# Optimization experiments

Measured on AMD Instinct MI355X. Metric: run time of the kernel, lower is better.

The kernel has to match this reference:

```python
import jax, jax.numpy as jnp
import numpy as np

HEADDIM = 128
CHUNK = 256


def _ssd_scan(x, dt, A, B, C, chunk):
    # x: (b,l,h,p)  dt: (b,l,h)  A: (h,)  B,C: (b,l,n)  (single group g=1 shared by all heads)
    b, l, h, p = x.shape
    n = B.shape[-1]
    nc = l // chunk
    dA = dt * A  # (b,l,h)
    xc = x.reshape(b, nc, chunk, h, p)
    dtc = dt.reshape(b, nc, chunk, h)
    dAc = dA.reshape(b, nc, chunk, h)
    Bc = B.reshape(b, nc, chunk, n)
    Cc = C.reshape(b, nc, chunk, n)
    cs = jnp.cumsum(dAc, axis=2)  # (b,nc,c,h) cumulative log-decay within chunk
    # intra-chunk quadratic part
    CB = jnp.einsum('bjin,bjkn->bjik', Cc, Bc)  # (b,nc,c,c)
    decay = jnp.exp(cs[:, :, :, None, :] - cs[:, :, None, :, :])  # (b,nc,i,k,h)
    mask = jnp.tril(jnp.ones((chunk, chunk), dtype=bool))
    decay = jnp.where(mask[None, None, :, :, None], decay, 0.0)
    y_intra = jnp.einsum('bjik,bjikh,bjkh,bjkhp->bjihp', CB, decay, dtc, xc)
    # per-chunk end states
    decay_states = jnp.exp(cs[:, :, -1:, :] - cs)  # (b,nc,c,h)
    states = jnp.einsum('bjkh,bjkh,bjkn,bjkhp->bjhnp', decay_states, dtc, Bc, xc)
    # recurrence across chunks: h_j = exp(sum dA_j) * h_{j-1} + states_j
    chunk_decay = jnp.exp(cs[:, :, -1, :])  # (b,nc,h)
    def step(carry, inp):
        s, d = inp
        new = carry * d[:, :, None, None] + s
        return new, carry  # emit state BEFORE this chunk
    init = jnp.zeros((b, h, n, p), x.dtype)
    _, prev = jax.lax.scan(step, init,
                           (states.transpose(1, 0, 2, 3, 4), chunk_decay.transpose(1, 0, 2)))
    prev = prev.transpose(1, 0, 2, 3, 4)  # (b,nc,h,n,p)
    y_inter = jnp.einsum('bjih,bjin,bjhnp->bjihp', jnp.exp(cs), Cc, prev)
    return (y_intra + y_inter).reshape(b, l, h, p)


def setup_inputs() -> dict:
    key = jax.random.key(0)
    k1, k2, k3, k4 = jax.random.split(key, 4)
    b, l, d_inner, nheads, d_state = 2, 4096, 2048, 16, 256
    x = jax.random.normal(k1, (b, l, d_inner), dtype=jnp.float32)
    BC = jax.random.normal(k2, (b, l, 2 * d_state), dtype=jnp.float32) * 0.1
    dt = jax.random.normal(k3, (b, l, 2 * nheads), dtype=jnp.float32) - 3.0
    A_log = jnp.zeros((nheads,), dtype=jnp.float32)
    D = jnp.ones((nheads,), dtype=jnp.float32)
    W_fcD = jax.random.normal(k4, (nheads, d_inner), dtype=jnp.float32) * 0.02
    return {"x": x, "BC": BC, "dt": dt, "A_log": A_log, "D": D, "W_fcD": W_fcD}


def reference(x, BC, dt, A_log, D, W_fcD):
    b, l, dim = x.shape
    h = A_log.shape[0]
    p = HEADDIM
    d_state = BC.shape[-1] // 2
    A = -jnp.exp(A_log)
    # bidirectional: concat forward stream with time-flipped backward stream along batch
    dt2 = jnp.concatenate((dt[:, :, :h], jnp.flip(dt[:, :, h:], axis=1)), axis=0)
    dt2 = jax.nn.softplus(dt2)
    x_og = x
    x2 = jnp.concatenate((x, jnp.flip(x, axis=1)), axis=0)
    BC2 = jnp.concatenate((BC, jnp.flip(BC, axis=1)), axis=0)
    B, C = BC2[..., :d_state], BC2[..., d_state:]
    y = _ssd_scan(x2.reshape(2 * b, l, h, p), dt2, A, B, C, CHUNK)
    y = y.reshape(2 * b, l, dim)
    y = jnp.roll(y, shift=1, axis=1).at[:, 0, :].set(0.0)
    y_fw, y_bw = y[:b], jnp.flip(y[b:], axis=1)
    gate = x_og @ W_fcD.T + D  # (b,l,h)
    y = y_fw + y_bw + x_og * jnp.repeat(gate, p, axis=-1)
    return y
```

## Files before the change

### kernel.cpp

```cpp
#include <hip/hip_runtime.h>
#include <stdint.h>

#define NB 2
#define SL 4096
#define NH 16
#define HD 128
#define DS 256
#define CK 256
#define NCH 16
#define NSQ 4
#define DI 2048

typedef unsigned short u16;
typedef unsigned int u32;
typedef __attribute__((ext_vector_type(8))) __bf16 bf16x8;
typedef __attribute__((ext_vector_type(4))) float f32x4;

__device__ __forceinline__ int tor(int dir, int t) { return dir ? (SL - 1 - t) : t; }

__device__ __forceinline__ u16 f2bf(float f) {
  u32 u = __float_as_uint(f);
  u = u + 0x7fffu + ((u >> 16) & 1u);
  return (u16)(u >> 16);
}
__device__ __forceinline__ float bf2f(u16 s) {
  return __uint_as_float(((u32)s) << 16);
}

__device__ __forceinline__ void gl_lds16(const u16* g, u16* l) {
  __builtin_amdgcn_global_load_lds((const __attribute__((address_space(1))) u32*)g,
                                   (__attribute__((address_space(3))) u32*)l, 16, 0, 0);
}

__device__ __forceinline__ void stage_tile(const u16* __restrict__ src, u16* lds,
                                           int lane, int w, int k0) {
  int sgrow = lane >> 2, sc = lane & 3;
  int r0 = w << 5;
  int ra = r0 + sgrow, rb = ra + 16;
  int kqa = (sc ^ ((ra >> 1) & 3)) << 3;
  int kqb = (sc ^ ((rb >> 1) & 3)) << 3;
  gl_lds16(src + (size_t)ra * 256 + k0 + kqa, lds + r0 * 32);
  gl_lds16(src + (size_t)rb * 256 + k0 + kqb, lds + (r0 + 16) * 32);
}

__device__ __forceinline__ bf16x8 frag(const u16* lds, int base_row, int m, int quad) {
  int row = base_row + m;
  return *(const bf16x8*)&lds[row * 32 + ((quad ^ ((row >> 1) & 3)) << 3)];
}

__device__ __forceinline__ void mfma16(const u16* As, const u16* Bs, int wi, int wp,
                                       int m, int quad, f32x4 acc[4][4]) {
  bf16x8 af[4], bv[4];
#pragma unroll
  for (int r = 0; r < 4; ++r) af[r] = frag(As, wi + (r << 4), m, quad);
#pragma unroll
  for (int c = 0; c < 4; ++c) bv[c] = frag(Bs, wp + (c << 4), m, quad);
#pragma unroll
  for (int r = 0; r < 4; ++r)
#pragma unroll
    for (int c = 0; c < 4; ++c)
      acc[r][c] = __builtin_amdgcn_mfma_f32_16x16x32_bf16(af[r], bv[c], acc[r][c], 0, 0, 0);
}

__global__ __launch_bounds__(256) void kprep(const float* __restrict__ dt,
                                             const float* __restrict__ A_log,
                                             float* __restrict__ csb,
                                             float* __restrict__ dtvb,
                                             float* __restrict__ cdecb) {
  int blk = blockIdx.x;
  int h = blk & 15, sj = blk >> 4;
  int s = sj >> 4, j = sj & 15;
  int b = s & 1, dir = s >> 1;
  int i = threadIdx.x;
  int to = tor(dir, j * CK + i);
  __shared__ float sbuf[CK];
  float a = -expf(A_log[h]);
  float raw = dt[((size_t)(b * SL + to)) * (2 * NH) + dir * NH + h];
  float sp = (raw > 20.f) ? raw : log1pf(expf(raw));
  sbuf[i] = sp * a;
  __syncthreads();
  for (int off = 1; off < CK; off <<= 1) {
    float v = (i >= off) ? sbuf[i - off] : 0.f;
    __syncthreads();
    sbuf[i] += v;
    __syncthreads();
  }
  float csv = sbuf[i];
  size_t base = ((size_t)sj * NH + h) * CK;
  csb[base + i] = csv;
  dtvb[base + i] = sp;
  if (i == CK - 1) cdecb[sj * NH + h] = expf(csv);
}

__global__ __launch_bounds__(256) void kcast(const float* __restrict__ BC,
                                             u16* __restrict__ Bbf,
                                             u16* __restrict__ Cbf) {
  int blk = blockIdx.x;
  int s = blk >> 12, t = blk & (SL - 1);
  int b = s & 1, dir = s >> 1;
  int tsrc = tor(dir, t);
  int tid = threadIdx.x;
  const float* src = BC + ((size_t)(b * SL + tsrc)) * (2 * DS);
  size_t dstb = ((size_t)s * SL + t) * DS;
  Bbf[dstb + tid] = f2bf(src[tid]);
  Cbf[dstb + tid] = f2bf(src[DS + tid]);
}

__global__ __launch_bounds__(256) void ktransB(const u16* __restrict__ Bbf,
                                               u16* __restrict__ BbfT) {
  int sj = blockIdx.x;
  int s = sj >> 4, j = sj & 15;
  __shared__ u16 T[64 * 264];
  int tid = threadIdx.x;
  const u16* src = Bbf + ((size_t)s * SL + j * CK) * DS;
  u16* dst = BbfT + (size_t)sj * DS * CK;
  int kr = tid >> 2, part = (tid & 3) * 64;
  for (int k0 = 0; k0 < CK; k0 += 64) {
    __syncthreads();
    {
      const uint4* gs = (const uint4*)(src + (size_t)(k0 + kr) * DS + part);
      uint4* tb = (uint4*)&T[kr * 264 + part];
#pragma unroll
      for (int q = 0; q < 8; ++q) tb[q] = gs[q];
    }
    __syncthreads();
    int n = tid;
    u16 col[64];
#pragma unroll
    for (int kq = 0; kq < 64; ++kq) col[kq] = T[kq * 264 + n];
    uint4* ds_ = (uint4*)(dst + (size_t)n * CK + k0);
#pragma unroll
    for (int q = 0; q < 8; ++q) {
      uint4 wv;
      wv.x = (u32)col[q * 8 + 0] | ((u32)col[q * 8 + 1] << 16);
      wv.y = (u32)col[q * 8 + 2] | ((u32)col[q * 8 + 3] << 16);
      wv.z = (u32)col[q * 8 + 4] | ((u32)col[q * 8 + 5] << 16);
      wv.w = (u32)col[q * 8 + 6] | ((u32)col[q * 8 + 7] << 16);
      ds_[q] = wv;
    }
  }
}

__global__ __launch_bounds__(256) void kxsT(const float* __restrict__ xg,
                                            const float* __restrict__ csb,
                                            const float* __restrict__ dtvb,
                                            u16* __restrict__ xsT) {
  int inst = blockIdx.x;
  int h = inst & 15, sj = inst >> 4;
  int s = sj >> 4, j = sj & 15;
  int b = s & 1, dir = s >> 1;
  int tid = threadIdx.x;
  __shared__ u16 Ls[128 * 40];
  size_t cbase = ((size_t)sj * NH + h) * CK;
  u16* dst = xsT + (size_t)inst * (128 * 256);
  int kk = tid >> 3;
  int pg = (tid & 7) * 16;
  int p2 = tid >> 1, half = tid & 1;
  for (int k0 = 0; k0 < CK; k0 += 32) {
    int kglob = k0 + kk;
    float sc_ = expf(-csb[cbase + kglob]) * dtvb[cbase + kglob];
    int t = tor(dir, j * CK + kglob);
    const float* src = xg + ((size_t)(b * SL + t)) * DI + h * HD + pg;
    float4 v0 = ((const float4*)src)[0];
    float4 v1 = ((const float4*)src)[1];
    float4 v2 = ((const float4*)src)[2];
    float4 v3 = ((const float4*)src)[3];
    float vv[16] = {v0.x, v0.y, v0.z, v0.w, v1.x, v1.y, v1.z, v1.w,
                    v2.x, v2.y, v2.z, v2.w, v3.x, v3.y, v3.z, v3.w};
    __syncthreads();
#pragma unroll
    for (int q = 0; q < 16; ++q) Ls[(pg + q) * 40 + kk] = f2bf(vv[q] * sc_);
    __syncthreads();
    uint4 w0 = *(const uint4*)&Ls[p2 * 40 + half * 16];
    uint4 w1 = *(const uint4*)&Ls[p2 * 40 + half * 16 + 8];
    *(uint4*)&dst[(size_t)p2 * 256 + k0 + half * 16] = w0;
    *(uint4*)&dst[(size_t)p2 * 256 + k0 + half * 16 + 8] = w1;
  }
}

__global__ __launch_bounds__(256) void kcb(const u16* __restrict__ Cbf,
                                           const u16* __restrict__ Bbf,
                                           u16* __restrict__ CBm) {
  int blk = blockIdx.x;
  int tri = blk % 3;
  int sj = blk / 3;
  int it0 = tri ? 128 : 0;
  int kt0 = (tri == 2) ? 128 : 0;
  int s = sj >> 4, j = sj & 15;
  __shared__ u16 As[128 * 32];
  __shared__ u16 Bs[128 * 32];
  int tid = threadIdx.x;
  int w = tid >> 6, lane = tid & 63;
  int wi = (w >> 1) << 6, wp = (w & 1) << 6;
  int m = lane & 15, quad = lane >> 4;
  const u16* Ab = Cbf + ((size_t)s * SL + j * CK + it0) * DS;
  const u16* Bb = Bbf + ((size_t)s * SL + j * CK + kt0) * DS;
  f32x4 zini = {0.f, 0.f, 0.f, 0.f};
  f32x4 acc[4][4];
#pragma unroll
  for (int r = 0; r < 4; ++r)
#pragma unroll
    for (int c = 0; c < 4; ++c) acc[r][c] = zini;
  for (int ks = 0; ks < 8; ++ks) {
    int k0 = ks << 5;
    stage_tile(Ab, As, lane, w, k0);
    stage_tile(Bb, Bs, lane, w, k0);
    __syncthreads();
    mfma16(As, Bs, wi, wp, m, quad, acc);
    __syncthreads();
  }
  int diag = (it0 == kt0);
  u16* dst = CBm + ((size_t)sj * CK + it0) * CK + kt0;
#pragma unroll
  for (int r = 0; r < 4; ++r)
#pragma unroll
    for (int rg = 0; rg < 4; ++rg) {
      int irow = wi + (r << 4) + (quad << 2) + rg;
#pragma unroll
      for (int c = 0; c < 4; ++c) {
        int kcol = wp + (c << 4) + m;
        float v = acc[r][c][rg];
        if (diag && kcol > irow) v = 0.f;
        dst[(size_t)irow * CK + kcol] = f2bf(v);
      }
    }
}

__global__ __launch_bounds__(256) void kstates(const u16* __restrict__ xsT,
                                               const u16* __restrict__ BbfT,
                                               const float* __restrict__ cdecb,
                                               u16* __restrict__ prevT) {
  int blk = blockIdx.x;
  int ntile = blk & 1;
  int inst = blk >> 1;
  int h = inst & 15, sj = inst >> 4;
  int nt0 = ntile << 7;
  __shared__ u16 As[128 * 32];
  __shared__ u16 Bs[128 * 32];
  int tid = threadIdx.x;
  int w = tid >> 6, lane = tid & 63;
  int wi = (w >> 1) << 6, wp = (w & 1) << 6;
  int m = lane & 15, quad = lane >> 4;
  const u16* Ab = xsT + (size_t)inst * (128 * 256);
  const u16* Bb = BbfT + ((size_t)sj * DS + nt0) * CK;
  f32x4 zini = {0.f, 0.f, 0.f, 0.f};
  f32x4 acc[4][4];
#pragma unroll
  for (int r = 0; r < 4; ++r)
#pragma unroll
    for (int c = 0; c < 4; ++c) acc[r][c] = zini;
  for (int ks = 0; ks < 8; ++ks) {
    int k0 = ks << 5;
    stage_tile(Ab, As, lane, w, k0);
    stage_tile(Bb, Bs, lane, w, k0);
    __syncthreads();
    mfma16(As, Bs, wi, wp, m, quad, acc);
    __syncthreads();
  }
  float scale = cdecb[sj * NH + h];
  u16* dst = prevT + (size_t)inst * (128 * 256) + nt0;
#pragma unroll
  for (int r = 0; r < 4; ++r)
#pragma unroll
    for (int rg = 0; rg < 4; ++rg) {
      int prow = wi + (r << 4) + (quad << 2) + rg;
#pragma unroll
      for (int c = 0; c < 4; ++c) {
        int ncol = wp + (c << 4) + m;
        dst[(size_t)prow * 256 + ncol] = f2bf(acc[r][c][rg] * scale);
      }
    }
}

__global__ __launch_bounds__(256) void kscan(u16* __restrict__ prevT,
                                             const float* __restrict__ cdecb) {
  int g = blockIdx.x * 256 + threadIdx.x;
  int n = g & 255;
  int p = (g >> 8) & 127;
  int h = (g >> 15) & 15;
  int s = g >> 19;
  size_t base = (((size_t)(s * 256 + h) * 128) + p) * 256 + n;
  const size_t stride = (size_t)NH * 128 * 256;
  float carry = 0.f;
  for (int j = 0; j < NCH; ++j) {
    size_t idx = base + (size_t)j * stride;
    float sv = bf2f(prevT[idx]);
    prevT[idx] = f2bf(carry);
    carry = carry * cdecb[(s * NCH + j) * NH + h] + sv;
  }
}

__global__ __launch_bounds__(256) void ky(const u16* __restrict__ CBm,
                                          const u16* __restrict__ Cbf,
                                          const u16* __restrict__ xsT,
                                          const u16* __restrict__ prevT,
                                          const float* __restrict__ csb,
                                          u16* __restrict__ ytmpb) {
  int blk = blockIdx.x;
  int itile = blk & 1;
  int inst = blk >> 1;
  int h = inst & 15, sj = inst >> 4;
  int s = sj >> 4, j = sj & 15;
  int it0 = itile << 7;
  __shared__ u16 As[128 * 32];
  __shared__ u16 Bs[128 * 32];
  int tid = threadIdx.x;
  int w = tid >> 6, lane = tid & 63;
  int wi = (w >> 1) << 6, wp = (w & 1) << 6;
  int m = lane & 15, quad = lane >> 4;

  const u16* Ai = CBm + ((size_t)sj * CK + it0) * CK;
  const u16* Ae = Cbf + ((size_t)s * SL + j * CK + it0) * DS;
  const u16* Bi = xsT + (size_t)inst * (128 * 256);
  const u16* Be = prevT + (size_t)inst * (128 * 256);

  int nIntra = itile ? 8 : 4;
  int nTot = nIntra + 8;

  f32x4 zini = {0.f, 0.f, 0.f, 0.f};
  f32x4 acc[4][4];
#pragma unroll
  for (int r = 0; r < 4; ++r)
#pragma unroll
    for (int c = 0; c < 4; ++c) acc[r][c] = zini;

  for (int ks = 0; ks < nTot; ++ks) {
    int intra = ks < nIntra;
    int k0 = (intra ? ks : ks - nIntra) << 5;
    const u16* Ab = intra ? Ai : Ae;
    const u16* Bb = intra ? Bi : Be;
    stage_tile(Ab, As, lane, w, k0);
    stage_tile(Bb, Bs, lane, w, k0);
    __syncthreads();
    mfma16(As, Bs, wi, wp, m, quad, acc);
    __syncthreads();
  }
  const float* csrow = csb + ((size_t)sj * NH + h) * CK + it0;
  u16* yb = ytmpb + ((size_t)s * SL + j * CK + it0) * DI + h * HD;
#pragma unroll
  for (int r = 0; r < 4; ++r)
#pragma unroll
    for (int rg = 0; rg < 4; ++rg) {
      int irow = wi + (r << 4) + (quad << 2) + rg;
      float esc = expf(csrow[irow]);
#pragma unroll
      for (int c = 0; c < 4; ++c) {
        int pcol = wp + (c << 4) + m;
        yb[(size_t)irow * DI + pcol] = f2bf(acc[r][c][rg] * esc);
      }
    }
}

__global__ __launch_bounds__(256) void kgate(const float* __restrict__ xg,
                                             const float* __restrict__ Wg,
                                             const float* __restrict__ Dg,
                                             float* __restrict__ gates) {
  int bid = blockIdx.x;
  int b = bid >> 8;
  int t0 = (bid & 255) << 4;
  __shared__ float Wl[16 * 256];
  int tid = threadIdx.x;
  int w = tid >> 6, lane = tid & 63;
  int c4 = lane << 2;

  float acc[4][16];
#pragma unroll
  for (int r = 0; r < 4; ++r)
#pragma unroll
    for (int h = 0; h < 16; ++h) acc[r][h] = 0.f;

  for (int i = 0; i < 8; ++i) {
    __syncthreads();
#pragma unroll
    for (int q = 0; q < 4; ++q) {
      int idx = q * 256 + tid;
      int h = idx >> 6;
      int c = (idx & 63) << 2;
      *(float4*)&Wl[h * 256 + c] = *(const float4*)&Wg[(size_t)h * DI + i * 256 + c];
    }
    __syncthreads();
    float4 Wf[16];
#pragma unroll
    for (int h = 0; h < 16; ++h) Wf[h] = *(const float4*)&Wl[h * 256 + c4];
#pragma unroll
    for (int r = 0; r < 4; ++r) {
      int t = t0 + (w << 2) + r;
      float4 xv = *(const float4*)&xg[((size_t)(b * SL + t)) * DI + i * 256 + c4];
#pragma unroll
      for (int h = 0; h < 16; ++h)
        acc[r][h] += xv.x * Wf[h].x + xv.y * Wf[h].y + xv.z * Wf[h].z + xv.w * Wf[h].w;
    }
  }
#pragma unroll
  for (int r = 0; r < 4; ++r)
#pragma unroll
    for (int h = 0; h < 16; ++h) {
      float v = acc[r][h];
      v += __shfl_xor(v, 32);
      v += __shfl_xor(v, 16);
      v += __shfl_xor(v, 8);
      v += __shfl_xor(v, 4);
      v += __shfl_xor(v, 2);
      v += __shfl_xor(v, 1);
      acc[r][h] = v;
    }
  if (lane == 0) {
#pragma unroll
    for (int r = 0; r < 4; ++r) {
      int t = t0 + (w << 2) + r;
      float* gdst = gates + ((size_t)(b * SL + t)) * NH;
#pragma unroll
      for (int h = 0; h < 16; ++h) gdst[h] = acc[r][h] + Dg[h];
    }
  }
}

__device__ __forceinline__ void unpk8(uint4 u, float* o) {
  o[0] = __uint_as_float(u.x << 16); o[1] = __uint_as_float(u.x & 0xffff0000u);
  o[2] = __uint_as_float(u.y << 16); o[3] = __uint_as_float(u.y & 0xffff0000u);
  o[4] = __uint_as_float(u.z << 16); o[5] = __uint_as_float(u.z & 0xffff0000u);
  o[6] = __uint_as_float(u.w << 16); o[7] = __uint_as_float(u.w & 0xffff0000u);
}

__global__ __launch_bounds__(256) void kstream(const float* __restrict__ xg,
                                               const float* __restrict__ gates,
                                               const u16* __restrict__ ytmpb,
                                               float* __restrict__ out) {
  int bid = blockIdx.x;
  int b = bid >> 10;
  int t0 = (bid & 1023) << 2;
  int tid = threadIdx.x;
  int d0 = tid << 3;
  int h8 = tid >> 4;
  const u16* fwbase = ytmpb + (size_t)b * SL * DI + d0;
  const u16* bwbase = ytmpb + (size_t)(2 + b) * SL * DI + d0;
#pragma unroll
  for (int r = 0; r < 4; ++r) {
    int t = t0 + r;
    size_t rowb = ((size_t)(b * SL + t)) * DI + d0;
    float4 x0 = *(const float4*)&xg[rowb];
    float4 x1 = *(const float4*)&xg[rowb + 4];
    float fy[8] = {0.f, 0.f, 0.f, 0.f, 0.f, 0.f, 0.f, 0.f};
    float by[8] = {0.f, 0.f, 0.f, 0.f, 0.f, 0.f, 0.f, 0.f};
    if (t > 0) unpk8(*(const uint4*)(fwbase + (size_t)(t - 1) * DI), fy);
    if (t < SL - 1) unpk8(*(const uint4*)(bwbase + (size_t)(SL - 2 - t) * DI), by);
    float g = gates[((size_t)(b * SL + t)) * NH + h8];
    float4 o0, o1;
    o0.x = fy[0] + by[0] + x0.x * g;
    o0.y = fy[1] + by[1] + x0.y * g;
    o0.z = fy[2] + by[2] + x0.z * g;
    o0.w = fy[3] + by[3] + x0.w * g;
    o1.x = fy[4] + by[4] + x1.x * g;
    o1.y = fy[5] + by[5] + x1.y * g;
    o1.z = fy[6] + by[6] + x1.z * g;
    o1.w = fy[7] + by[7] + x1.w * g;
    *(float4*)&out[rowb] = o0;
    *(float4*)&out[rowb + 4] = o1;
  }
}

extern "C" void kernel_launch(void* const* d_in, const int* in_sizes, int n_in,
                              void* d_out, int out_size, void* d_ws, size_t ws_size,
                              hipStream_t stream) {
  (void)in_sizes; (void)n_in; (void)out_size; (void)ws_size;
  const float* x     = (const float*)d_in[0];
  const float* BC    = (const float*)d_in[1];
  const float* dt    = (const float*)d_in[2];
  const float* A_log = (const float*)d_in[3];
  const float* Dg    = (const float*)d_in[4];
  const float* W     = (const float*)d_in[5];
  float* out = (float*)d_out;

  char* p = (char*)d_ws;
  float* cs    = (float*)p; p += (size_t)NSQ * NCH * NH * CK * 4;
  float* dtv   = (float*)p; p += (size_t)NSQ * NCH * NH * CK * 4;
  float* cdec  = (float*)p; p += (size_t)NSQ * NCH * NH * 4;
  float* gates = (float*)p; p += (size_t)NB * SL * NH * 4;
  u16* Bbf    = (u16*)p;    p += (size_t)NSQ * SL * DS * 2;
  u16* Cbf    = (u16*)p;    p += (size_t)NSQ * SL * DS * 2;
  u16* BbfT   = (u16*)p;    p += (size_t)NSQ * NCH * DS * CK * 2;
  u16* CBm    = (u16*)p;    p += (size_t)NSQ * NCH * CK * CK * 2;
  u16* xsT    = (u16*)p;    p += (size_t)NSQ * NCH * NH * HD * CK * 2;
  u16* prevT  = (u16*)p;    p += (size_t)NSQ * NCH * NH * HD * DS * 2;
  u16* ytmpb  = (u16*)p;    p += (size_t)NSQ * SL * DI * 2;

  hipLaunchKernelGGL(kgate,   dim3(NB * SL / 16),        dim3(256), 0, stream, x, W, Dg, gates);
  hipLaunchKernelGGL(kprep,   dim3(NSQ * NCH * NH),      dim3(CK),  0, stream, dt, A_log, cs, dtv, cdec);
  hipLaunchKernelGGL(kcast,   dim3(NSQ * SL),            dim3(256), 0, stream, BC, Bbf, Cbf);
  hipLaunchKernelGGL(ktransB, dim3(NSQ * NCH),           dim3(256), 0, stream, Bbf, BbfT);
  hipLaunchKernelGGL(kxsT,    dim3(NSQ * NCH * NH),      dim3(256), 0, stream, x, cs, dtv, xsT);
  hipLaunchKernelGGL(kcb,     dim3(NSQ * NCH * 3),       dim3(256), 0, stream, Cbf, Bbf, CBm);
  hipLaunchKernelGGL(kstates, dim3(NSQ * NCH * NH * 2),  dim3(256), 0, stream, xsT, BbfT, cdec, prevT);
  hipLaunchKernelGGL(kscan,   dim3(NSQ * NH * HD * DS / 256), dim3(256), 0, stream, prevT, cdec);
  hipLaunchKernelGGL(ky,      dim3(NSQ * NCH * NH * 2),  dim3(256), 0, stream, CBm, Cbf, xsT, prevT, cs, ytmpb);
  hipLaunchKernelGGL(kstream, dim3(NB * SL / 4),         dim3(256), 0, stream, x, gates, ytmpb, out);
}
```

Baseline: 389.4 us.

## Vectorize BC cast, split transpose, double-buffer kcb, merge tiles in kstates/ky

The BC cast kernel now converts eight floats per thread with 16-byte loads and stores, eight timesteps per block. The B transpose is split into four k-slice blocks for more parallelism. kcb double-buffers its LDS tiles so the next load overlaps the MFMA work. kstates and ky now use 512-thread blocks that cover the full 256-wide tile, so the shared operand is staged once instead of twice. This cuts grid size and redundant global loads, at the cost of fewer blocks and an uneven causal-skip split in ky.

```diff
diff --git a/kernel.cpp b/kernel.cpp
--- a/kernel.cpp
+++ b/kernel.cpp
@@ -41,6 +41,14 @@
   int kqb = (sc ^ ((rb >> 1) & 3)) << 3;
   gl_lds16(src + (size_t)ra * 256 + k0 + kqa, lds + r0 * 32);
   gl_lds16(src + (size_t)rb * 256 + k0 + kqb, lds + (r0 + 16) * 32);
+}
+
+__device__ __forceinline__ void stage_half(const u16* __restrict__ src, u16* lds,
+                                           int lane, int w, int k0) {
+  int row = (w << 4) + (lane >> 2);
+  int sc = lane & 3;
+  int kq = (sc ^ ((row >> 1) & 3)) << 3;
+  gl_lds16(src + (size_t)row * 256 + k0 + kq, lds + (w << 4) * 32);
 }
 
 __device__ __forceinline__ bf16x8 frag(const u16* lds, int base_row, int m, int quad) {
@@ -96,48 +104,59 @@
                                              u16* __restrict__ Bbf,
                                              u16* __restrict__ Cbf) {
   int blk = blockIdx.x;
-  int s = blk >> 12, t = blk & (SL - 1);
+  int s = blk >> 9, tg = blk & 511;
   int b = s & 1, dir = s >> 1;
-  int tsrc = tor(dir, t);
-  int tid = threadIdx.x;
-  const float* src = BC + ((size_t)(b * SL + tsrc)) * (2 * DS);
-  size_t dstb = ((size_t)s * SL + t) * DS;
-  Bbf[dstb + tid] = f2bf(src[tid]);
-  Cbf[dstb + tid] = f2bf(src[DS + tid]);
+  int tid = threadIdx.x;
+  int rr = tid >> 6, q = tid & 63;
+  int isC = q >> 5, qq = q & 31;
+#pragma unroll
+  for (int it = 0; it < 2; ++it) {
+    int t = tg * 8 + it * 4 + rr;
+    int tsrc = tor(dir, t);
+    const float* src = BC + ((size_t)(b * SL + tsrc)) * (2 * DS) + q * 8;
+    float4 v0 = ((const float4*)src)[0];
+    float4 v1 = ((const float4*)src)[1];
+    uint4 wv;
+    wv.x = (u32)f2bf(v0.x) | ((u32)f2bf(v0.y) << 16);
+    wv.y = (u32)f2bf(v0.z) | ((u32)f2bf(v0.w) << 16);
+    wv.z = (u32)f2bf(v1.x) | ((u32)f2bf(v1.y) << 16);
+    wv.w = (u32)f2bf(v1.z) | ((u32)f2bf(v1.w) << 16);
+    u16* dstb = (isC ? Cbf : Bbf) + ((size_t)s * SL + t) * DS + qq * 8;
+    *(uint4*)dstb = wv;
+  }
 }
 
 __global__ __launch_bounds__(256) void ktransB(const u16* __restrict__ Bbf,
                                                u16* __restrict__ BbfT) {
-  int sj = blockIdx.x;
+  int blk = blockIdx.x;
+  int kslice = blk & 3, sj = blk >> 2;
+  int k0 = kslice << 6;
   int s = sj >> 4, j = sj & 15;
   __shared__ u16 T[64 * 264];
   int tid = threadIdx.x;
   const u16* src = Bbf + ((size_t)s * SL + j * CK) * DS;
   u16* dst = BbfT + (size_t)sj * DS * CK;
   int kr = tid >> 2, part = (tid & 3) * 64;
-  for (int k0 = 0; k0 < CK; k0 += 64) {
-    __syncthreads();
-    {
-      const uint4* gs = (const uint4*)(src + (size_t)(k0 + kr) * DS + part);
-      uint4* tb = (uint4*)&T[kr * 264 + part];
-#pragma unroll
-      for (int q = 0; q < 8; ++q) tb[q] = gs[q];
-    }
-    __syncthreads();
-    int n = tid;
-    u16 col[64];
-#pragma unroll
-    for (int kq = 0; kq < 64; ++kq) col[kq] = T[kq * 264 + n];
-    uint4* ds_ = (uint4*)(dst + (size_t)n * CK + k0);
-#pragma unroll
-    for (int q = 0; q < 8; ++q) {
-      uint4 wv;
-      wv.x = (u32)col[q * 8 + 0] | ((u32)col[q * 8 + 1] << 16);
-      wv.y = (u32)col[q * 8 + 2] | ((u32)col[q * 8 + 3] << 16);
-      wv.z = (u32)col[q * 8 + 4] | ((u32)col[q * 8 + 5] << 16);
-      wv.w = (u32)col[q * 8 + 6] | ((u32)col[q * 8 + 7] << 16);
-      ds_[q] = wv;
-    }
+  {
+    const uint4* gs = (const uint4*)(src + (size_t)(k0 + kr) * DS + part);
+    uint4* tb = (uint4*)&T[kr * 264 + part];
+#pragma unroll
+    for (int q = 0; q < 8; ++q) tb[q] = gs[q];
+  }
+  __syncthreads();
+  int n = tid;
+  u16 col[64];
+#pragma unroll
+  for (int kq = 0; kq < 64; ++kq) col[kq] = T[kq * 264 + n];
+  uint4* ds_ = (uint4*)(dst + (size_t)n * CK + k0);
+#pragma unroll
+  for (int q = 0; q < 8; ++q) {
+    uint4 wv;
+    wv.x = (u32)col[q * 8 + 0] | ((u32)col[q * 8 + 1] << 16);
+    wv.y = (u32)col[q * 8 + 2] | ((u32)col[q * 8 + 3] << 16);
+    wv.z = (u32)col[q * 8 + 4] | ((u32)col[q * 8 + 5] << 16);
+    wv.w = (u32)col[q * 8 + 6] | ((u32)col[q * 8 + 7] << 16);
+    ds_[q] = wv;
   }
 }
 
@@ -187,8 +206,8 @@
   int it0 = tri ? 128 : 0;
   int kt0 = (tri == 2) ? 128 : 0;
   int s = sj >> 4, j = sj & 15;
-  __shared__ u16 As[128 * 32];
-  __shared__ u16 Bs[128 * 32];
+  __shared__ u16 As[2][128 * 32];
+  __shared__ u16 Bs[2][128 * 32];
   int tid = threadIdx.x;
   int w = tid >> 6, lane = tid & 63;
   int wi = (w >> 1) << 6, wp = (w & 1) << 6;
@@ -201,13 +220,19 @@
   for (int r = 0; r < 4; ++r)
 #pragma unroll
     for (int c = 0; c < 4; ++c) acc[r][c] = zini;
+  stage_tile(Ab, As[0], lane, w, 0);
+  stage_tile(Bb, Bs[0], lane, w, 0);
+  __syncthreads();
+  int cur = 0;
   for (int ks = 0; ks < 8; ++ks) {
-    int k0 = ks << 5;
-    stage_tile(Ab, As, lane, w, k0);
-    stage_tile(Bb, Bs, lane, w, k0);
-    __syncthreads();
-    mfma16(As, Bs, wi, wp, m, quad, acc);
-    __syncthreads();
+    if (ks + 1 < 8) {
+      int k1 = (ks + 1) << 5;
+      stage_tile(Ab, As[cur ^ 1], lane, w, k1);
+      stage_tile(Bb, Bs[cur ^ 1], lane, w, k1);
+    }
+    mfma16(As[cur], Bs[cur], wi, wp, m, quad, acc);
+    __syncthreads();
+    cur ^= 1;
   }
   int diag = (it0 == kt0);
   u16* dst = CBm + ((size_t)sj * CK + it0) * CK + kt0;
@@ -226,23 +251,21 @@
     }
 }
 
-__global__ __launch_bounds__(256) void kstates(const u16* __restrict__ xsT,
+__global__ __launch_bounds__(512) void kstates(const u16* __restrict__ xsT,
                                                const u16* __restrict__ BbfT,
                                                const float* __restrict__ cdecb,
                                                u16* __restrict__ prevT) {
-  int blk = blockIdx.x;
-  int ntile = blk & 1;
-  int inst = blk >> 1;
+  int inst = blockIdx.x;
   int h = inst & 15, sj = inst >> 4;
-  int nt0 = ntile << 7;
   __shared__ u16 As[128 * 32];
-  __shared__ u16 Bs[128 * 32];
+  __shared__ u16 Bs[256 * 32];
   int tid = threadIdx.x;
   int w = tid >> 6, lane = tid & 63;
-  int wi = (w >> 1) << 6, wp = (w & 1) << 6;
+  int wi = (w >> 2) << 6;
+  int wp = (w & 3) << 6;
   int m = lane & 15, quad = lane >> 4;
   const u16* Ab = xsT + (size_t)inst * (128 * 256);
-  const u16* Bb = BbfT + ((size_t)sj * DS + nt0) * CK;
+  const u16* Bb = BbfT + (size_t)sj * DS * CK;
   f32x4 zini = {0.f, 0.f, 0.f, 0.f};
   f32x4 acc[4][4];
 #pragma unroll
@@ -251,14 +274,14 @@
     for (int c = 0; c < 4; ++c) acc[r][c] = zini;
   for (int ks = 0; ks < 8; ++ks) {
     int k0 = ks << 5;
-    stage_tile(Ab, As, lane, w, k0);
+    stage_half(Ab, As, lane, w, k0);
     stage_tile(Bb, Bs, lane, w, k0);
     __syncthreads();
     mfma16(As, Bs, wi, wp, m, quad, acc);
     __syncthreads();
   }
   float scale = cdecb[sj * NH + h];
-  u16* dst = prevT + (size_t)inst * (128 * 256) + nt0;
+  u16* dst = prevT + (size_t)inst * (128 * 256);
 #pragma unroll
   for (int r = 0; r < 4; ++r)
 #pragma unroll
@@ -290,33 +313,28 @@
   }
 }
 
-__global__ __launch_bounds__(256) void ky(const u16* __restrict__ CBm,
+__global__ __launch_bounds__(512) void ky(const u16* __restrict__ CBm,
                                           const u16* __restrict__ Cbf,
                                           const u16* __restrict__ xsT,
                                           const u16* __restrict__ prevT,
                                           const float* __restrict__ csb,
                                           u16* __restrict__ ytmpb) {
-  int blk = blockIdx.x;
-  int itile = blk & 1;
-  int inst = blk >> 1;
+  int inst = blockIdx.x;
   int h = inst & 15, sj = inst >> 4;
   int s = sj >> 4, j = sj & 15;
-  int it0 = itile << 7;
-  __shared__ u16 As[128 * 32];
+  __shared__ u16 As[256 * 32];
   __shared__ u16 Bs[128 * 32];
   int tid = threadIdx.x;
   int w = tid >> 6, lane = tid & 63;
-  int wi = (w >> 1) << 6, wp = (w & 1) << 6;
+  int wi = (w >> 1) << 6;
+  int wp = (w & 1) << 6;
   int m = lane & 15, quad = lane >> 4;
 
-  const u16* Ai = CBm + ((size_t)sj * CK + it0) * CK;
-  const u16* Ae = Cbf + ((size_t)s * SL + j * CK + it0) * DS;
+  const u16* Ai = CBm + (size_t)sj * CK * CK;
+  const u16* Ae = Cbf + ((size_t)s * SL + j * CK) * DS;
   const u16* Bi = xsT + (size_t)inst * (128 * 256);
   const u16* Be = prevT + (size_t)inst * (128 * 256);
 
-  int nIntra = itile ? 8 : 4;
-  int nTot = nIntra + 8;
-
   f32x4 zini = {0.f, 0.f, 0.f, 0.f};
   f32x4 acc[4][4];
 #pragma unroll
@@ -324,19 +342,22 @@
 #pragma unroll
     for (int c = 0; c < 4; ++c) acc[r][c] = zini;
 
-  for (int ks = 0; ks < nTot; ++ks) {
-    int intra = ks < nIntra;
-    int k0 = (intra ? ks : ks - nIntra) << 5;
-    const u16* Ab = intra ? Ai : Ae;
-    const u16* Bb = intra ? Bi : Be;
-    stage_tile(Ab, As, lane, w, k0);
-    stage_tile(Bb, Bs, lane, w, k0);
-    __syncthreads();
-    mfma16(As, Bs, wi, wp, m, quad, acc);
-    __syncthreads();
-  }
-  const float* csrow = csb + ((size_t)sj * NH + h) * CK + it0;
-  u16* yb = ytmpb + ((size_t)s * SL + j * CK + it0) * DI + h * HD;
+  for (int ks = 0; ks < 16; ++ks) {
+    int intra = ks < 8;
+    int k0 = (intra ? ks : ks - 8) << 5;
+    if (intra) {
+      if (ks < 4 || w >= 4) stage_tile(Ai, As, lane, w, k0);
+    } else {
+      stage_tile(Ae, As, lane, w, k0);
+    }
+    stage_half(intra ? Bi : Be, Bs, lane, w, k0);
+    __syncthreads();
+    if (!intra || ks < 4 || wi >= 128)
+      mfma16(As, Bs, wi, wp, m, quad, acc);
+    __syncthreads();
+  }
+  const float* csrow = csb + ((size_t)sj * NH + h) * CK;
+  u16* yb = ytmpb + ((size_t)s * SL + j * CK) * DI + h * HD;
 #pragma unroll
   for (int r = 0; r < 4; ++r)
 #pragma unroll
@@ -486,12 +507,12 @@
 
   hipLaunchKernelGGL(kgate,   dim3(NB * SL / 16),        dim3(256), 0, stream, x, W, Dg, gates);
   hipLaunchKernelGGL(kprep,   dim3(NSQ * NCH * NH),      dim3(CK),  0, stream, dt, A_log, cs, dtv, cdec);
-  hipLaunchKernelGGL(kcast,   dim3(NSQ * SL),            dim3(256), 0, stream, BC, Bbf, Cbf);
-  hipLaunchKernelGGL(ktransB, dim3(NSQ * NCH),           dim3(256), 0, stream, Bbf, BbfT);
+  hipLaunchKernelGGL(kcast,   dim3(NSQ * SL / 8),        dim3(256), 0, stream, BC, Bbf, Cbf);
+  hipLaunchKernelGGL(ktransB, dim3(NSQ * NCH * 4),       dim3(256), 0, stream, Bbf, BbfT);
   hipLaunchKernelGGL(kxsT,    dim3(NSQ * NCH * NH),      dim3(256), 0, stream, x, cs, dtv, xsT);
   hipLaunchKernelGGL(kcb,     dim3(NSQ * NCH * 3),       dim3(256), 0, stream, Cbf, Bbf, CBm);
-  hipLaunchKernelGGL(kstates, dim3(NSQ * NCH * NH * 2),  dim3(256), 0, stream, xsT, BbfT, cdec, prevT);
+  hipLaunchKernelGGL(kstates, dim3(NSQ * NCH * NH),      dim3(512), 0, stream, xsT, BbfT, cdec, prevT);
   hipLaunchKernelGGL(kscan,   dim3(NSQ * NH * HD * DS / 256), dim3(256), 0, stream, prevT, cdec);
-  hipLaunchKernelGGL(ky,      dim3(NSQ * NCH * NH * 2),  dim3(256), 0, stream, CBm, Cbf, xsT, prevT, cs, ytmpb);
+  hipLaunchKernelGGL(ky,      dim3(NSQ * NCH * NH),      dim3(512), 0, stream, CBm, Cbf, xsT, prevT, cs, ytmpb);
   hipLaunchKernelGGL(kstream, dim3(NB * SL / 4),         dim3(256), 0, stream, x, gates, ytmpb, out);
 }
```

After: 383.1 us. No clear change (-1.6%).
